# Kernel tuning notes

Hardware: AMD Instinct MI355X
Metric: run time of the kernel (lower is better)

The kernel has to match this reference:

```python
import jax, jax.numpy as jnp
import numpy as np


def setup_inputs() -> dict:
    key = jax.random.key(0)
    ks = jax.random.split(key, 9)
    B, T, C = 4, 2048, 2048
    E, I, SI = 8, 1408, 5632
    s = lambda k, shape, fan_in: jax.random.normal(k, shape, jnp.float32) * (fan_in ** -0.5)
    return {
        "x": jax.random.normal(ks[0], (B, T, C), jnp.float32),
        "gate_w": s(ks[1], (C, E), C),                  # router: x @ gate_w -> [N,E]
        "expert_gate_w": s(ks[2], (E, C, I), C),        # stacked gate_proj weights
        "expert_up_w": s(ks[3], (E, C, I), C),          # stacked up_proj weights
        "expert_down_w": s(ks[4], (E, I, C), I),        # stacked down_proj weights
        "shared_gate_w": s(ks[5], (C, SI), C),
        "shared_up_w": s(ks[6], (C, SI), C),
        "shared_down_w": s(ks[7], (SI, C), SI),
        "shared_expert_gate_w": s(ks[8], (C, 1), C),
        "top_k": 4,
    }


def reference(x, gate_w, expert_gate_w, expert_up_w, expert_down_w,
              shared_gate_w, shared_up_w, shared_down_w, shared_expert_gate_w, top_k):
    B, T, C = x.shape
    E = gate_w.shape[1]
    xf = x.reshape(-1, C)                      # [N, C]
    N = xf.shape[0]

    # --- router: softmax (fp32) -> top-k -> renormalize ---
    logits = xf @ gate_w                       # [N, E]
    probs = jax.nn.softmax(logits.astype(jnp.float32), axis=-1)
    w, idx = jax.lax.top_k(probs, top_k)       # [N, k]
    w = w / jnp.sum(w, axis=-1, keepdims=True)

    # dense combine gates [N, E]: zero for non-selected experts (equivalent to
    # the torch dispatch/sort/combine: each token gets weight w_k on expert idx_k)
    gates = jnp.zeros((N, E), jnp.float32).at[jnp.arange(N)[:, None], idx].add(w)

    # --- per-expert SwiGLU MLP, accumulated via scan over experts ---
    def step(acc, ew):
        wg, wu, wd, g = ew                     # wg/wu: [C,I], wd: [I,C], g: [N]
        h = jax.nn.silu(xf @ wg) * (xf @ wu)   # [N, I]
        return acc + g[:, None] * (h @ wd), None

    routed, _ = jax.lax.scan(
        step, jnp.zeros_like(xf),
        (expert_gate_w, expert_up_w, expert_down_w, gates.T))

    # --- shared expert with sigmoid gate ---
    shared = (jax.nn.silu(xf @ shared_gate_w) * (xf @ shared_up_w)) @ shared_down_w
    sg = jax.nn.sigmoid(xf @ shared_expert_gate_w)   # [N, 1]

    return (routed + sg * shared).reshape(B, T, C)
```

## Files before the change

### kernel.cpp

```cpp
#include <hip/hip_runtime.h>
#include <hip/hip_bf16.h>
#include <stdint.h>


typedef float f32x4 __attribute__((ext_vector_type(4)));
typedef int   i32x4 __attribute__((ext_vector_type(4)));
typedef __hip_bfloat16 bf16;

#define DEV __device__ __forceinline__

DEV void mfma16(f32x4& c, const i32x4& a, const i32x4& b) {
    asm("v_mfma_f32_16x16x32_bf16 %0, %1, %2, %0" : "+v"(c) : "v"(a), "v"(b));
}

template<int ROWS>
DEV void stage(const bf16* gtile, long ldK, char* lds, int tid) {
    const int wid = tid >> 6, lane = tid & 63;
    const int swz = ((lane & 7) ^ (lane >> 3)) << 4;
    constexpr int NISS = (ROWS * 128) / 4096;
    #pragma unroll
    for (int i = 0; i < NISS; i++) {
        const int o = i * 4096 + wid * 1024;
        const int row = (o >> 7) + (lane >> 3);
        const char* ga = (const char*)gtile + (long)row * (ldK * 2) + swz;
        __builtin_amdgcn_global_load_lds(
            (const __attribute__((address_space(1))) void*)ga,
            (__attribute__((address_space(3))) void*)(lds + o), 16, 0, 0);
    }
}

template<int ROWS>
DEV void stage_idx(const char* base, const long* roff, int ktb, char* lds,
                   int tid, int swz) {
    const int wid = tid >> 6;
    constexpr int NISS = (ROWS * 128) / 4096;
    #pragma unroll
    for (int i = 0; i < NISS; i++) {
        const int o = i * 4096 + wid * 1024;
        const char* ga = base + roff[i] + ktb + swz;
        __builtin_amdgcn_global_load_lds(
            (const __attribute__((address_space(1))) void*)ga,
            (__attribute__((address_space(3))) void*)(lds + o), 16, 0, 0);
    }
}

DEV i32x4 ldsfrag(const char* lds, int row, int kbyte) {
    const int off = (row << 7) + (kbyte ^ ((row & 7) << 4));
    return *(const i32x4*)(lds + off);
}

__global__ __launch_bounds__(256) void tcvt(const float* __restrict__ src,
        bf16* __restrict__ dst, int Cd, long dld, long sz, long dz) {
    __shared__ float t[64][65];
    const long z = blockIdx.z;
    src += z * sz; dst += z * dz;
    const int cb = blockIdx.x * 64, rb = blockIdx.y * 64;
    const int tx = threadIdx.x & 63, ty = threadIdx.x >> 6;
    #pragma unroll
    for (int i = 0; i < 16; i++) {
        const int r = ty + i * 4;
        t[r][tx] = src[(long)(rb + r) * Cd + cb + tx];
    }
    __syncthreads();
    #pragma unroll
    for (int i = 0; i < 16; i++) {
        const int c = ty + i * 4;
        dst[(long)(cb + c) * dld + rb + tx] = __float2bfloat16(t[tx][c]);
    }
}

__global__ __launch_bounds__(256) void cvtx(const float* __restrict__ x,
        bf16* __restrict__ xb, long n4) {
    long i = (long)blockIdx.x * blockDim.x + threadIdx.x;
    const long stride = (long)gridDim.x * blockDim.x;
    for (; i < n4; i += stride) {
        const float4 v = ((const float4*)x)[i];
        union { bf16 h[4]; ushort4 u; } cu;
        cu.h[0] = __float2bfloat16(v.x); cu.h[1] = __float2bfloat16(v.y);
        cu.h[2] = __float2bfloat16(v.z); cu.h[3] = __float2bfloat16(v.w);
        ((ushort4*)xb)[i] = cu.u;
    }
}

__global__ __launch_bounds__(256) void router(const float* __restrict__ x,
        const float* __restrict__ gw, const float* __restrict__ segw,
        int* __restrict__ tidx, float* __restrict__ tw,
        float* __restrict__ sg, int C) {
    const int lane = threadIdx.x & 63;
    const long t = (long)blockIdx.x * 4 + (threadIdx.x >> 6);
    const float* xr = x + t * C;
    float a[9];
    #pragma unroll
    for (int e = 0; e < 9; e++) a[e] = 0.f;
    for (int c = lane; c < C; c += 64) {
        const float xv = xr[c];
        const float4* g4 = (const float4*)(gw + (long)c * 8);
        const float4 g0 = g4[0], g1 = g4[1];
        a[0] += xv * g0.x; a[1] += xv * g0.y; a[2] += xv * g0.z; a[3] += xv * g0.w;
        a[4] += xv * g1.x; a[5] += xv * g1.y; a[6] += xv * g1.z; a[7] += xv * g1.w;
        a[8] += xv * segw[c];
    }
    #pragma unroll
    for (int e = 0; e < 9; e++) {
        #pragma unroll
        for (int o = 32; o; o >>= 1) a[e] += __shfl_xor(a[e], o, 64);
    }
    if (lane == 0) {
        float m = a[0];
        #pragma unroll
        for (int e = 1; e < 8; e++) m = fmaxf(m, a[e]);
        float p[8]; float s = 0.f;
        #pragma unroll
        for (int e = 0; e < 8; e++) { p[e] = expf(a[e] - m); s += p[e]; }
        #pragma unroll
        for (int e = 0; e < 8; e++) p[e] /= s;
        bool used[8] = {false,false,false,false,false,false,false,false};
        float wsum = 0.f; int idx[4]; float wv[4];
        for (int k = 0; k < 4; k++) {
            float best = -1.f; int bi = 0;
            for (int e = 0; e < 8; e++)
                if (!used[e] && p[e] > best) { best = p[e]; bi = e; }
            used[bi] = true; idx[k] = bi; wv[k] = best; wsum += best;
        }
        int4 iv; float4 wv4;
        iv.x = idx[0]; iv.y = idx[1]; iv.z = idx[2]; iv.w = idx[3];
        wv4.x = wv[0] / wsum; wv4.y = wv[1] / wsum;
        wv4.z = wv[2] / wsum; wv4.w = wv[3] / wsum;
        ((int4*)tidx)[t] = iv;
        ((float4*)tw)[t] = wv4;
        sg[t] = 1.f / (1.f + expf(-a[8]));
    }
}

__global__ __launch_bounds__(256) void build_lists(const int* __restrict__ tidx,
        const float* __restrict__ tw, int* __restrict__ tok,
        float* __restrict__ wl, int* __restrict__ cnt, int N) {
    const int e = blockIdx.x;
    const int tid = threadIdx.x;
    const int per = N / 256;
    __shared__ int csum[256];
    int c = 0;
    for (int i = 0; i < per; i++) {
        const int4 id4 = ((const int4*)tidx)[tid * per + i];
        if (id4.x == e || id4.y == e || id4.z == e || id4.w == e) c++;
    }
    csum[tid] = c;
    __syncthreads();
    for (int o = 1; o < 256; o <<= 1) {
        const int v = (tid >= o) ? csum[tid - o] : 0;
        __syncthreads();
        csum[tid] += v;
        __syncthreads();
    }
    int pos = csum[tid] - c;
    if (tid == 255) cnt[e] = csum[255];
    for (int i = 0; i < per; i++) {
        const int t = tid * per + i;
        const int4   id4 = ((const int4*)tidx)[t];
        const float4 w4  = ((const float4*)tw)[t];
        float w = 0.f; int hit = 0;
        if      (id4.x == e) { w = w4.x; hit = 1; }
        else if (id4.y == e) { w = w4.y; hit = 1; }
        else if (id4.z == e) { w = w4.z; hit = 1; }
        else if (id4.w == e) { w = w4.w; hit = 1; }
        if (hit) { tok[(long)e * N + pos] = t; wl[(long)e * N + pos] = w; pos++; }
    }
}

__global__ __launch_bounds__(256) void dual_gemm(const bf16* __restrict__ A,
        const int* __restrict__ tok, long tokz,
        const int* __restrict__ cnt, int Mfix,
        const bf16* __restrict__ BG0, const bf16* __restrict__ BU0, long bz,
        bf16* __restrict__ H0, long hld, long hz,
        const float* __restrict__ sc0, long scz, int K) {
    __shared__ __align__(128) char Al[16384];
    __shared__ __align__(128) char Gl[8192];
    __shared__ __align__(128) char Ul[8192];
    const int z = blockIdx.z;
    const int Me = cnt ? cnt[z] : Mfix;
    const long m0 = (long)blockIdx.x * 128;
    if (m0 >= Me) return;
    const int* ridx = tok ? tok + (long)z * tokz : nullptr;
    const bf16* BG = BG0 + (long)z * bz;
    const bf16* BU = BU0 + (long)z * bz;
    bf16* H = H0 + (long)z * hz;
    const float* sc = sc0 + (long)z * scz;
    const int tid = threadIdx.x, lane = tid & 63, wid = tid >> 6;
    const long n0 = (long)blockIdx.y * 64;
    const int wm = (wid >> 1) * 64, wn = (wid & 1) * 32;
    const int l15 = lane & 15, lhi = lane >> 4;
    const int swz = ((lane & 7) ^ (lane >> 3)) << 4;
    long roffA[4];
    #pragma unroll
    for (int i = 0; i < 4; i++) {
        const int rit = ((i * 4096 + wid * 1024) >> 7) + (lane >> 3);
        int g = (int)m0 + rit;
        if (ridx) g = ridx[g < Me ? g : Me - 1];
        roffA[i] = (long)g * (K * 2);
    }
    f32x4 ag[4][2] = {}; f32x4 au[4][2] = {};
    for (int kt = 0; kt < K; kt += 64) {
        stage_idx<128>((const char*)A, roffA, kt * 2, Al, tid, swz);
        stage<64>(BG + n0 * K + kt, (long)K, Gl, tid);
        stage<64>(BU + n0 * K + kt, (long)K, Ul, tid);
        __syncthreads();
        #pragma unroll
        for (int ks = 0; ks < 2; ks++) {
            const int kb = ks * 64 + lhi * 16;
            i32x4 af[4], bg[2], bu[2];
            #pragma unroll
            for (int mi = 0; mi < 4; mi++) af[mi] = ldsfrag(Al, wm + mi * 16 + l15, kb);
            #pragma unroll
            for (int ni = 0; ni < 2; ni++) {
                bg[ni] = ldsfrag(Gl, wn + ni * 16 + l15, kb);
                bu[ni] = ldsfrag(Ul, wn + ni * 16 + l15, kb);
            }
            #pragma unroll
            for (int mi = 0; mi < 4; mi++) {
                #pragma unroll
                for (int ni = 0; ni < 2; ni++) {
                    mfma16(ag[mi][ni], af[mi], bg[ni]);
                    mfma16(au[mi][ni], af[mi], bu[ni]);
                }
            }
        }
        __syncthreads();
    }
    asm volatile("s_nop 7\n\ts_nop 7\n\ts_nop 7");
    #pragma unroll
    for (int mi = 0; mi < 4; mi++) {
        #pragma unroll
        for (int r = 0; r < 4; r++) {
            const int pos = (int)m0 + wm + mi * 16 + lhi * 4 + r;
            if (pos < Me) {
                const float s = sc[pos];
                #pragma unroll
                for (int ni = 0; ni < 2; ni++) {
                    const float gv = ag[mi][ni][r], uv = au[mi][ni][r];
                    const float h = (gv / (1.f + expf(-gv))) * uv * s;
                    H[(long)pos * hld + n0 + wn + ni * 16 + l15] = __float2bfloat16(h);
                }
            }
        }
    }
}

__global__ __launch_bounds__(256) void gemm_down(const bf16* __restrict__ A,
        const bf16* __restrict__ BT, float* __restrict__ C,
        const int* __restrict__ ridx, const int* __restrict__ cntp, int Mfix,
        int K, long ldc, int beta) {
    __shared__ __align__(128) char Al[16384];
    __shared__ __align__(128) char Bl[16384];
    const int Me = cntp ? *cntp : Mfix;
    const long m0 = (long)blockIdx.y * 128;
    if (m0 >= Me) return;
    const int tid = threadIdx.x, lane = tid & 63, wid = tid >> 6;
    const long n0 = (long)blockIdx.x * 128;
    const int wm = (wid >> 1) * 64, wn = (wid & 1) * 64;
    const int l15 = lane & 15, lhi = lane >> 4;
    f32x4 acc[4][4] = {};
    for (int kt = 0; kt < K; kt += 64) {
        stage<128>(A  + m0 * K + kt, (long)K, Al, tid);
        stage<128>(BT + n0 * K + kt, (long)K, Bl, tid);
        __syncthreads();
        #pragma unroll
        for (int ks = 0; ks < 2; ks++) {
            const int kb = ks * 64 + lhi * 16;
            i32x4 af[4], bfr[4];
            #pragma unroll
            for (int mi = 0; mi < 4; mi++) af[mi]  = ldsfrag(Al, wm + mi * 16 + l15, kb);
            #pragma unroll
            for (int ni = 0; ni < 4; ni++) bfr[ni] = ldsfrag(Bl, wn + ni * 16 + l15, kb);
            #pragma unroll
            for (int mi = 0; mi < 4; mi++) {
                #pragma unroll
                for (int ni = 0; ni < 4; ni++) mfma16(acc[mi][ni], af[mi], bfr[ni]);
            }
        }
        __syncthreads();
    }
    asm volatile("s_nop 7\n\ts_nop 7\n\ts_nop 7");
    #pragma unroll
    for (int mi = 0; mi < 4; mi++) {
        #pragma unroll
        for (int r = 0; r < 4; r++) {
            const int pos = (int)m0 + wm + mi * 16 + lhi * 4 + r;
            if (pos < Me) {
                const long orow = ridx ? (long)ridx[pos] : (long)pos;
                #pragma unroll
                for (int ni = 0; ni < 4; ni++) {
                    const long ci = orow * ldc + n0 + wn + ni * 16 + l15;
                    float v = acc[mi][ni][r];
                    if (beta) v += C[ci];
                    C[ci] = v;
                }
            }
        }
    }
}

extern "C" void kernel_launch(void* const* d_in, const int* in_sizes, int n_in,
                              void* d_out, int out_size, void* d_ws, size_t ws_size,
                              hipStream_t stream) {
    const int N = 8192, Cdim = 2048, E = 8, I = 1408, SI = 5632;

    const float* x    = (const float*)d_in[0];
    const float* gw   = (const float*)d_in[1];
    const float* egw  = (const float*)d_in[2];
    const float* euw  = (const float*)d_in[3];
    const float* edw  = (const float*)d_in[4];
    const float* sgw  = (const float*)d_in[5];
    const float* suw  = (const float*)d_in[6];
    const float* sdw  = (const float*)d_in[7];
    const float* segw = (const float*)d_in[8];
    float* out = (float*)d_out;

    char* ws = (char*)d_ws;
    size_t off = 0;
    auto alloc = [&](size_t bytes) { char* p = ws + off; off += (bytes + 255) & ~(size_t)255; return p; };

    bf16*  xb   = (bf16*) alloc((size_t)N * Cdim * 2);
    int*   tidx = (int*)  alloc((size_t)N * 4 * 4);
    float* tw   = (float*)alloc((size_t)N * 4 * 4);
    float* sg   = (float*)alloc((size_t)N * 4);
    int*   tok  = (int*)  alloc((size_t)E * N * 4);
    float* wl   = (float*)alloc((size_t)E * N * 4);
    int*   cnt  = (int*)  alloc(256);

    const size_t WSLOT = (size_t)SI * Cdim * 2;
    bf16* Wa = (bf16*)alloc(WSLOT);
    bf16* Wb = (bf16*)alloc(WSLOT);
    bf16* Wc = (bf16*)alloc(WSLOT);
    bf16* Hc = (bf16*)alloc((size_t)N * SI * 2);
    if (off > ws_size) return;

    cvtx<<<4096, 256, 0, stream>>>(x, xb, (long)N * Cdim / 4);
    router<<<N / 4, 256, 0, stream>>>(x, gw, segw, tidx, tw, sg, Cdim);
    build_lists<<<E, 256, 0, stream>>>(tidx, tw, tok, wl, cnt, N);

    tcvt<<<dim3(SI / 64, Cdim / 64, 1), 256, 0, stream>>>(sgw, Wa, SI, (long)Cdim, 0, 0);
    tcvt<<<dim3(SI / 64, Cdim / 64, 1), 256, 0, stream>>>(suw, Wb, SI, (long)Cdim, 0, 0);
    tcvt<<<dim3(Cdim / 64, SI / 64, 1), 256, 0, stream>>>(sdw, Wc, Cdim, (long)SI, 0, 0);
    dual_gemm<<<dim3(N / 128, SI / 64, 1), 256, 0, stream>>>(xb,
            nullptr, 0, nullptr, N, Wa, Wb, 0, Hc, (long)SI, 0, sg, 0, Cdim);
    gemm_down<<<dim3(Cdim / 128, N / 128), 256, 0, stream>>>(Hc, Wc, out,
            nullptr, nullptr, N, SI, (long)Cdim, 0);

    for (int b = 0; b < 2; b++) {
        const int e0 = b * 4;
        tcvt<<<dim3(I / 64, Cdim / 64, 4), 256, 0, stream>>>(
                egw + (long)e0 * Cdim * I, Wa, I, (long)Cdim,
                (long)Cdim * I, (long)I * Cdim);
        tcvt<<<dim3(I / 64, Cdim / 64, 4), 256, 0, stream>>>(
                euw + (long)e0 * Cdim * I, Wb, I, (long)Cdim,
                (long)Cdim * I, (long)I * Cdim);
        tcvt<<<dim3(Cdim / 64, I / 64, 4), 256, 0, stream>>>(
                edw + (long)e0 * I * Cdim, Wc, Cdim, (long)I,
                (long)I * Cdim, (long)Cdim * I);
        dual_gemm<<<dim3(N / 128, I / 64, 4), 256, 0, stream>>>(xb,
                tok + (long)e0 * N, (long)N, cnt + e0, 0,
                Wa, Wb, (long)I * Cdim,
                Hc, (long)I, (long)N * I,
                wl + (long)e0 * N, (long)N, Cdim);
        for (int z = 0; z < 4; z++) {
            gemm_down<<<dim3(Cdim / 128, N / 128), 256, 0, stream>>>(
                    Hc + (long)z * N * I, Wc + (long)z * Cdim * I, out,
                    tok + (long)(e0 + z) * N, cnt + e0 + z, 0,
                    I, (long)Cdim, 1);
        }
    }
}
```

Before: 1.642 ms.

## Replace dual GEMM with 512-thread double-buffered 256x128 tile kernel

The SwiGLU gate/up GEMM kernel now uses 256x128 output tiles computed by 8 waves instead of 128x64 tiles from 4 waves. Each K-step is split into four phases, and the next tile's global-to-LDS loads are prefetched into a second LDS buffer while MFMAs run on the current one. Synchronisation uses manual vmcnt waits, raw barriers and s_setprio around the MFMA bursts. Larger tiles raise operand reuse and the prefetch hides load latency, at the cost of 128KB of LDS per block, which limits the CU to one resident block. There are also fewer blocks for small expert token counts.

```diff
diff --git a/kernel.cpp b/kernel.cpp
--- a/kernel.cpp
+++ b/kernel.cpp
@@ -9,8 +9,20 @@
 
 #define DEV __device__ __forceinline__
 
+#define BARRIER() do { asm volatile("" ::: "memory"); \
+    __builtin_amdgcn_s_barrier(); asm volatile("" ::: "memory"); } while (0)
+#define WAITV0 asm volatile("s_waitcnt vmcnt(0)" ::: "memory")
+#define WAITV2 asm volatile("s_waitcnt vmcnt(2)" ::: "memory")
+#define WAITV4 asm volatile("s_waitcnt vmcnt(4)" ::: "memory")
+
 DEV void mfma16(f32x4& c, const i32x4& a, const i32x4& b) {
     asm("v_mfma_f32_16x16x32_bf16 %0, %1, %2, %0" : "+v"(c) : "v"(a), "v"(b));
+}
+
+DEV void g2l(const char* ga, char* ldst) {
+    __builtin_amdgcn_global_load_lds(
+        (const __attribute__((address_space(1))) void*)ga,
+        (__attribute__((address_space(3))) void*)ldst, 16, 0, 0);
 }
 
 template<int ROWS>
@@ -22,25 +34,7 @@
     for (int i = 0; i < NISS; i++) {
         const int o = i * 4096 + wid * 1024;
         const int row = (o >> 7) + (lane >> 3);
-        const char* ga = (const char*)gtile + (long)row * (ldK * 2) + swz;
-        __builtin_amdgcn_global_load_lds(
-            (const __attribute__((address_space(1))) void*)ga,
-            (__attribute__((address_space(3))) void*)(lds + o), 16, 0, 0);
-    }
-}
-
-template<int ROWS>
-DEV void stage_idx(const char* base, const long* roff, int ktb, char* lds,
-                   int tid, int swz) {
-    const int wid = tid >> 6;
-    constexpr int NISS = (ROWS * 128) / 4096;
-    #pragma unroll
-    for (int i = 0; i < NISS; i++) {
-        const int o = i * 4096 + wid * 1024;
-        const char* ga = base + roff[i] + ktb + swz;
-        __builtin_amdgcn_global_load_lds(
-            (const __attribute__((address_space(1))) void*)ga,
-            (__attribute__((address_space(3))) void*)(lds + o), 16, 0, 0);
+        g2l((const char*)gtile + (long)row * (ldK * 2) + swz, lds + o);
     }
 }
 
@@ -167,68 +161,140 @@
     }
 }
 
-__global__ __launch_bounds__(256) void dual_gemm(const bf16* __restrict__ A,
+__global__ __launch_bounds__(512, 2) void dual8(const bf16* __restrict__ A,
         const int* __restrict__ tok, long tokz,
         const int* __restrict__ cnt, int Mfix,
         const bf16* __restrict__ BG0, const bf16* __restrict__ BU0, long bz,
         bf16* __restrict__ H0, long hld, long hz,
         const float* __restrict__ sc0, long scz, int K) {
-    __shared__ __align__(128) char Al[16384];
-    __shared__ __align__(128) char Gl[8192];
-    __shared__ __align__(128) char Ul[8192];
+    __shared__ __align__(128) char Al[2][32768];
+    __shared__ __align__(128) char Gl[2][16384];
+    __shared__ __align__(128) char Ul[2][16384];
     const int z = blockIdx.z;
     const int Me = cnt ? cnt[z] : Mfix;
-    const long m0 = (long)blockIdx.x * 128;
+    const long m0 = (long)blockIdx.x * 256;
     if (m0 >= Me) return;
     const int* ridx = tok ? tok + (long)z * tokz : nullptr;
     const bf16* BG = BG0 + (long)z * bz;
     const bf16* BU = BU0 + (long)z * bz;
     bf16* H = H0 + (long)z * hz;
     const float* sc = sc0 + (long)z * scz;
+    const long n0 = (long)blockIdx.y * 128;
     const int tid = threadIdx.x, lane = tid & 63, wid = tid >> 6;
-    const long n0 = (long)blockIdx.y * 64;
-    const int wm = (wid >> 1) * 64, wn = (wid & 1) * 32;
+    const int wm = (wid >> 2) * 128, wn = (wid & 3) * 32;
     const int l15 = lane & 15, lhi = lane >> 4;
     const int swz = ((lane & 7) ^ (lane >> 3)) << 4;
+    const long Kb = (long)K * 2;
+
     long roffA[4];
     #pragma unroll
-    for (int i = 0; i < 4; i++) {
-        const int rit = ((i * 4096 + wid * 1024) >> 7) + (lane >> 3);
-        int g = (int)m0 + rit;
+    for (int r = 0; r < 4; r++) {
+        int g = (int)m0 + r * 64 + wid * 8 + (lane >> 3);
         if (ridx) g = ridx[g < Me ? g : Me - 1];
-        roffA[i] = (long)g * (K * 2);
-    }
-    f32x4 ag[4][2] = {}; f32x4 au[4][2] = {};
-    for (int kt = 0; kt < K; kt += 64) {
-        stage_idx<128>((const char*)A, roffA, kt * 2, Al, tid, swz);
-        stage<64>(BG + n0 * K + kt, (long)K, Gl, tid);
-        stage<64>(BU + n0 * K + kt, (long)K, Ul, tid);
-        __syncthreads();
-        #pragma unroll
-        for (int ks = 0; ks < 2; ks++) {
-            const int kb = ks * 64 + lhi * 16;
-            i32x4 af[4], bg[2], bu[2];
-            #pragma unroll
-            for (int mi = 0; mi < 4; mi++) af[mi] = ldsfrag(Al, wm + mi * 16 + l15, kb);
-            #pragma unroll
-            for (int ni = 0; ni < 2; ni++) {
-                bg[ni] = ldsfrag(Gl, wn + ni * 16 + l15, kb);
-                bu[ni] = ldsfrag(Ul, wn + ni * 16 + l15, kb);
-            }
-            #pragma unroll
-            for (int mi = 0; mi < 4; mi++) {
-                #pragma unroll
-                for (int ni = 0; ni < 2; ni++) {
-                    mfma16(ag[mi][ni], af[mi], bg[ni]);
-                    mfma16(au[mi][ni], af[mi], bu[ni]);
-                }
-            }
-        }
-        __syncthreads();
-    }
+        roffA[r] = (long)g * Kb;
+    }
+    long roffB[2];
+    #pragma unroll
+    for (int r = 0; r < 2; r++)
+        roffB[r] = (n0 + r * 64 + wid * 8 + (lane >> 3)) * Kb;
+
+    const int NT = K / 64;
+    #pragma unroll
+    for (int r = 0; r < 4; r++)
+        g2l((const char*)A + roffA[r] + swz, &Al[0][r * 8192 + wid * 1024]);
+    #pragma unroll
+    for (int r = 0; r < 2; r++)
+        g2l((const char*)BG + roffB[r] + swz, &Gl[0][r * 8192 + wid * 1024]);
+    #pragma unroll
+    for (int r = 0; r < 2; r++)
+        g2l((const char*)BU + roffB[r] + swz, &Ul[0][r * 8192 + wid * 1024]);
+    WAITV0;
+    BARRIER();
+
+    f32x4 aG[8][2] = {}; f32x4 aU[8][2] = {};
+
+    for (int t = 0; t < NT; ++t) {
+        const int p = t & 1;
+        const long ktb = (long)(t + 1) * 128;
+        const bool pf = (t + 1 < NT);
+        char* An = Al[p ^ 1]; char* Gn = Gl[p ^ 1]; char* Un = Ul[p ^ 1];
+        const char* Ac = Al[p]; const char* Gc = Gl[p]; const char* Uc = Ul[p];
+        i32x4 af[8], bf2[2];
+
+        #pragma unroll
+        for (int mi = 0; mi < 8; mi++) af[mi] = ldsfrag(Ac, wm + mi * 16 + l15, lhi * 16);
+        #pragma unroll
+        for (int ni = 0; ni < 2; ni++) bf2[ni] = ldsfrag(Gc, wn + ni * 16 + l15, lhi * 16);
+        if (pf) {
+            g2l((const char*)A + roffA[0] + ktb + swz, An + wid * 1024);
+            g2l((const char*)A + roffA[1] + ktb + swz, An + 8192 + wid * 1024);
+        }
+        BARRIER();
+        __builtin_amdgcn_s_setprio(1);
+        #pragma unroll
+        for (int mi = 0; mi < 8; mi++)
+            #pragma unroll
+            for (int ni = 0; ni < 2; ni++) mfma16(aG[mi][ni], af[mi], bf2[ni]);
+        __builtin_amdgcn_s_setprio(0);
+        BARRIER();
+
+        #pragma unroll
+        for (int mi = 0; mi < 8; mi++) af[mi] = ldsfrag(Ac, wm + mi * 16 + l15, 64 + lhi * 16);
+        #pragma unroll
+        for (int ni = 0; ni < 2; ni++) bf2[ni] = ldsfrag(Gc, wn + ni * 16 + l15, 64 + lhi * 16);
+        if (pf) {
+            g2l((const char*)A + roffA[2] + ktb + swz, An + 16384 + wid * 1024);
+            g2l((const char*)A + roffA[3] + ktb + swz, An + 24576 + wid * 1024);
+        }
+        BARRIER();
+        __builtin_amdgcn_s_setprio(1);
+        #pragma unroll
+        for (int mi = 0; mi < 8; mi++)
+            #pragma unroll
+            for (int ni = 0; ni < 2; ni++) mfma16(aG[mi][ni], af[mi], bf2[ni]);
+        __builtin_amdgcn_s_setprio(0);
+        WAITV4;
+        BARRIER();
+
+        #pragma unroll
+        for (int mi = 0; mi < 8; mi++) af[mi] = ldsfrag(Ac, wm + mi * 16 + l15, lhi * 16);
+        #pragma unroll
+        for (int ni = 0; ni < 2; ni++) bf2[ni] = ldsfrag(Uc, wn + ni * 16 + l15, lhi * 16);
+        if (pf) {
+            g2l((const char*)BG + roffB[0] + ktb + swz, Gn + wid * 1024);
+            g2l((const char*)BG + roffB[1] + ktb + swz, Gn + 8192 + wid * 1024);
+        }
+        BARRIER();
+        __builtin_amdgcn_s_setprio(1);
+        #pragma unroll
+        for (int mi = 0; mi < 8; mi++)
+            #pragma unroll
+            for (int ni = 0; ni < 2; ni++) mfma16(aU[mi][ni], af[mi], bf2[ni]);
+        __builtin_amdgcn_s_setprio(0);
+        BARRIER();
+
+        #pragma unroll
+        for (int mi = 0; mi < 8; mi++) af[mi] = ldsfrag(Ac, wm + mi * 16 + l15, 64 + lhi * 16);
+        #pragma unroll
+        for (int ni = 0; ni < 2; ni++) bf2[ni] = ldsfrag(Uc, wn + ni * 16 + l15, 64 + lhi * 16);
+        if (pf) {
+            g2l((const char*)BU + roffB[0] + ktb + swz, Un + wid * 1024);
+            g2l((const char*)BU + roffB[1] + ktb + swz, Un + 8192 + wid * 1024);
+        }
+        BARRIER();
+        __builtin_amdgcn_s_setprio(1);
+        #pragma unroll
+        for (int mi = 0; mi < 8; mi++)
+            #pragma unroll
+            for (int ni = 0; ni < 2; ni++) mfma16(aU[mi][ni], af[mi], bf2[ni]);
+        __builtin_amdgcn_s_setprio(0);
+        WAITV2;
+        BARRIER();
+    }
+
     asm volatile("s_nop 7\n\ts_nop 7\n\ts_nop 7");
     #pragma unroll
-    for (int mi = 0; mi < 4; mi++) {
+    for (int mi = 0; mi < 8; mi++) {
         #pragma unroll
         for (int r = 0; r < 4; r++) {
             const int pos = (int)m0 + wm + mi * 16 + lhi * 4 + r;
@@ -236,7 +302,7 @@
                 const float s = sc[pos];
                 #pragma unroll
                 for (int ni = 0; ni < 2; ni++) {
-                    const float gv = ag[mi][ni][r], uv = au[mi][ni][r];
+                    const float gv = aG[mi][ni][r], uv = aU[mi][ni][r];
                     const float h = (gv / (1.f + expf(-gv))) * uv * s;
                     H[(long)pos * hld + n0 + wn + ni * 16 + l15] = __float2bfloat16(h);
                 }
@@ -341,7 +407,7 @@
     tcvt<<<dim3(SI / 64, Cdim / 64, 1), 256, 0, stream>>>(sgw, Wa, SI, (long)Cdim, 0, 0);
     tcvt<<<dim3(SI / 64, Cdim / 64, 1), 256, 0, stream>>>(suw, Wb, SI, (long)Cdim, 0, 0);
     tcvt<<<dim3(Cdim / 64, SI / 64, 1), 256, 0, stream>>>(sdw, Wc, Cdim, (long)SI, 0, 0);
-    dual_gemm<<<dim3(N / 128, SI / 64, 1), 256, 0, stream>>>(xb,
+    dual8<<<dim3(N / 256, SI / 128, 1), 512, 0, stream>>>(xb,
             nullptr, 0, nullptr, N, Wa, Wb, 0, Hc, (long)SI, 0, sg, 0, Cdim);
     gemm_down<<<dim3(Cdim / 128, N / 128), 256, 0, stream>>>(Hc, Wc, out,
             nullptr, nullptr, N, SI, (long)Cdim, 0);
@@ -357,11 +423,13 @@
         tcvt<<<dim3(Cdim / 64, I / 64, 4), 256, 0, stream>>>(
                 edw + (long)e0 * I * Cdim, Wc, Cdim, (long)I,
                 (long)I * Cdim, (long)Cdim * I);
-        dual_gemm<<<dim3(N / 128, I / 64, 4), 256, 0, stream>>>(xb,
+
+        dual8<<<dim3(N / 256, I / 128, 4), 512, 0, stream>>>(xb,
                 tok + (long)e0 * N, (long)N, cnt + e0, 0,
                 Wa, Wb, (long)I * Cdim,
                 Hc, (long)I, (long)N * I,
                 wl + (long)e0 * N, (long)N, Cdim);
+
         for (int z = 0; z < 4; z++) {
             gemm_down<<<dim3(Cdim / 128, N / 128), 256, 0, stream>>>(
                     Hc + (long)z * N * I, Wc + (long)z * Cdim * I, out,
```

Measured after the change: 2.082 ms. 1.27x slower.
